# Performance work log

Hardware: AMD Instinct MI355X
Metric: run time of the kernel (lower is better)

The kernel has to match this reference:

```python
import jax, jax.numpy as jnp
import numpy as np

B, S, H, E, ID, ON, RF = 256, 512, 512, 128, 8192, 32, 32
RNN_IN = H + E + 1 + ON  # weighted + embedded + rate + online


def setup_inputs() -> dict:
    key = jax.random.key(0)
    ks = jax.random.split(key, 24)
    n = lambda k, sh, s=0.05: (jax.random.normal(k, sh, jnp.float32) * s)
    inp = {
        'input_id': jax.random.randint(ks[0], (B, 1), 0, ID),
        'input_rate': jax.random.uniform(ks[1], (B, 1), jnp.float32),
        'hidden': n(ks[2], (1, B, H), 1.0),
        'encoder_outputs': n(ks[3], (S, B, H), 1.0),
        'attn_mask': jax.random.randint(ks[4], (B, S), 0, 2).astype(jnp.float32),
        'pre_grid': jnp.zeros((B, 1), jnp.float32),
        'next_grid': jnp.zeros((B, 1), jnp.float32),
        'constraint_vec': jax.random.randint(ks[5], (B, ID), 0, 2).astype(jnp.float32),
        'pro_features': jnp.zeros((B, 8), jnp.float32),
        'online_features': n(ks[6], (B, ON), 1.0),
        'rid_features': n(ks[7], (B, RF), 1.0),
        # learned parameters
        'emb_id': n(ks[8], (ID, E)),
        'trans': n(ks[9], (ID, ID)),              # transition_matrix param
        'v_w': n(ks[10], (1, H)),                  # attention v (no bias)
        'attn_gate_w': n(ks[11], (H, 2 * H)),
        'attn_gate_b': jnp.zeros((H,), jnp.float32),
        'W_ih': n(ks[12], (3 * H, RNN_IN)),
        'W_hh': n(ks[13], (3 * H, H)),
        'b_ih': jnp.zeros((3 * H,), jnp.float32),
        'b_hh': jnp.zeros((3 * H,), jnp.float32),
        'gate_w': n(ks[14], (ID, ID)),             # Linear(id_size,id_size) of gate
        'gate_b': jnp.zeros((ID,), jnp.float32),
        'fc_id_w': n(ks[15], (ID, H)),
        'fc_id_b': jnp.zeros((ID,), jnp.float32),
        'tandem_w': n(ks[16], (H, E + H)),
        'tandem_b': jnp.zeros((H,), jnp.float32),
        'rate_w': n(ks[17], (1, H + RF)),
        'rate_b': jnp.zeros((1,), jnp.float32),
    }
    return inp


def reference(input_id, input_rate, hidden, encoder_outputs, attn_mask, pre_grid,
              next_grid, constraint_vec, pro_features, online_features, rid_features,
              emb_id, trans, v_w, attn_gate_w, attn_gate_b, W_ih, W_hh, b_ih, b_hh,
              gate_w, gate_b, fc_id_w, fc_id_b, tandem_w, tandem_b, rate_w, rate_b):
    h = hidden[0]                                  # [B,H]
    emb = emb_id[input_id[:, 0]]                   # [B,E] (dropout is eval no-op)

    # --- gated additive attention ---
    eo = jnp.transpose(encoder_outputs, (1, 0, 2))          # [B,S,H]
    hb = jnp.broadcast_to(h[:, None, :], eo.shape)          # [B,S,H]
    g = jax.nn.sigmoid(jnp.concatenate([hb, eo], -1) @ attn_gate_w.T + attn_gate_b)
    energy = jnp.tanh(g * hb + (1.0 - g) * eo)              # [B,S,H]
    att = jnp.squeeze(energy @ v_w.T, -1)                   # [B,S]
    att = jnp.where(attn_mask == 0, jnp.float32(-1e10), att)
    a = jax.nn.softmax(att, axis=1)
    weighted = jnp.einsum('bs,bsh->bh', a, eo)              # [B,H]

    # --- GRU cell (torch gate order r,z,n) ---
    rnn_in = jnp.concatenate([weighted, emb, input_rate, online_features], -1)
    gx = rnn_in @ W_ih.T + b_ih
    gh = h @ W_hh.T + b_hh
    r = jax.nn.sigmoid(gx[:, :H] + gh[:, :H])
    z = jax.nn.sigmoid(gx[:, H:2 * H] + gh[:, H:2 * H])
    nn_ = jnp.tanh(gx[:, 2 * H:] + r * gh[:, 2 * H:])
    h_new = (1.0 - z) * nn_ + z * h                          # [B,H]

    # --- gated transition matrix + masked log-softmax ---
    T = jax.nn.sigmoid(trans @ gate_w.T + gate_b)           # [ID,ID]
    logits = (h_new @ fc_id_w.T + fc_id_b) @ T              # [B,ID]
    maxes = jnp.max(logits, axis=1, keepdims=True) + 1e-5
    x_exp = jnp.exp(logits - maxes) * constraint_vec
    prediction_id = jnp.log(x_exp / jnp.sum(x_exp, axis=1, keepdims=True))

    # --- tandem rate head ---
    max_id = jnp.argmax(prediction_id, axis=1)
    id_emb = emb_id[max_id]
    rate_in = jax.nn.relu(jnp.concatenate([id_emb, h_new], -1) @ tandem_w.T + tandem_b)
    prediction_rate = jax.nn.sigmoid(
        jnp.concatenate([rate_in, rid_features], -1) @ rate_w.T + rate_b)
    return prediction_id, prediction_rate, h_new[None]
```

## Files before the change

### kernel.cpp

```cpp
#include <hip/hip_runtime.h>
#include <stdint.h>
#include <math.h>

#define B_    256
#define S_    512
#define H_    512
#define E_    128
#define ID_   8192
#define ON_   32
#define RF_   32
#define RIN_  673

typedef __attribute__((ext_vector_type(8))) short short8;
typedef __attribute__((ext_vector_type(4))) float f32x4;

__device__ __forceinline__ unsigned short f2bf(float x) {
    unsigned int u = __builtin_bit_cast(unsigned int, x);
    u += 0x7fffu + ((u >> 16) & 1u);
    return (unsigned short)(u >> 16);
}
__device__ __forceinline__ float bf2f(unsigned short v) {
    return __builtin_bit_cast(float, ((unsigned int)v) << 16);
}
__device__ __forceinline__ float sigf(float x) { return 1.0f / (1.0f + expf(-x)); }

__device__ __forceinline__ void async16(const void* g, void* l) {
    __builtin_amdgcn_global_load_lds((const __attribute__((address_space(1))) void*)g,
                                     (__attribute__((address_space(3))) void*)l, 16, 0, 0);
}

__global__ __launch_bounds__(256) void split_contig(const float* __restrict__ src,
        unsigned short* __restrict__ hi, unsigned short* __restrict__ lo, long long n4)
{
    long long i = (long long)blockIdx.x * 256 + threadIdx.x;
    if (i >= n4) return;
    float4 v = ((const float4*)src)[i];
    ushort4 h, l;
    h.x = f2bf(v.x); l.x = f2bf(v.x - bf2f(h.x));
    h.y = f2bf(v.y); l.y = f2bf(v.y - bf2f(h.y));
    h.z = f2bf(v.z); l.z = f2bf(v.z - bf2f(h.z));
    h.w = f2bf(v.w); l.w = f2bf(v.w - bf2f(h.w));
    ((ushort4*)hi)[i] = h;
    ((ushort4*)lo)[i] = l;
}

__global__ __launch_bounds__(256) void split_strided(const float* __restrict__ src,
        unsigned short* __restrict__ hi, unsigned short* __restrict__ lo,
        int rows, int cols, int stride, int coloff)
{
    int i = blockIdx.x * 256 + threadIdx.x;
    if (i >= rows * cols) return;
    int r = i / cols, c = i % cols;
    float v = src[(size_t)r * stride + coloff + c];
    unsigned short h = f2bf(v);
    hi[i] = h;
    lo[i] = f2bf(v - bf2f(h));
}

template<int BIAS , int ACT , int OSPLIT >
__global__ __launch_bounds__(256, 2) void gemm_split(
        const unsigned short* __restrict__ Ah, const unsigned short* __restrict__ Al,
        const unsigned short* __restrict__ Bh, const unsigned short* __restrict__ Bl,
        float* __restrict__ Cf, unsigned short* __restrict__ Ch, unsigned short* __restrict__ Cl,
        const float* __restrict__ bias, int M, int N, int K, int group_m)
{
    __shared__ short lds[2][16384];

    int num_m = M >> 7, num_n = N >> 7;
    int pid = blockIdx.x;
    int gsize = group_m * num_n;
    int gid = pid / gsize;
    int first_m = gid * group_m;
    int gsz = min(group_m, num_m - first_m);
    int bm = first_m + (pid % gsz);
    int bn = (pid % gsize) / gsz;
    int m0 = bm << 7, n0 = bn << 7;

    int tid = threadIdx.x;
    int w = tid >> 6, L = tid & 63;
    int wm = w & 1, wn = w >> 1;

    int ci0 = w * 128 + L;
    int ci1 = ci0 + 64;
    int row0 = ci0 >> 2, q0 = (ci0 & 3) ^ ((ci0 >> 3) & 3);
    int row1 = ci1 >> 2, q1 = (ci1 & 3) ^ ((ci1 >> 3) & 3);
    size_t aoff0 = (size_t)(m0 + row0) * K + q0 * 8;
    size_t aoff1 = (size_t)(m0 + row1) * K + q1 * 8;
    size_t boff0 = (size_t)(n0 + row0) * K + q0 * 8;
    size_t boff1 = (size_t)(n0 + row1) * K + q1 * 8;

    int r15 = L & 15;
    int qp = (L >> 4) ^ ((L >> 1) & 3);
    int fA = (wm * 64 + r15) * 32 + qp * 8;
    int fB = (wn * 64 + r15) * 32 + qp * 8;

    auto stage = [&](int buf) {
        short* l = &lds[buf][0];
        async16(Ah + aoff0, &l[ci0 * 8]);
        async16(Ah + aoff1, &l[ci1 * 8]);
        async16(Al + aoff0, &l[4096 + ci0 * 8]);
        async16(Al + aoff1, &l[4096 + ci1 * 8]);
        async16(Bh + boff0, &l[8192 + ci0 * 8]);
        async16(Bh + boff1, &l[8192 + ci1 * 8]);
        async16(Bl + boff0, &l[12288 + ci0 * 8]);
        async16(Bl + boff1, &l[12288 + ci1 * 8]);
        aoff0 += 32; aoff1 += 32; boff0 += 32; boff1 += 32;
    };

    f32x4 acc[4][4] = {};
    int nk = K >> 5;
    int cur = 0;

    stage(0);

    for (int t = 0; t < nk; ++t) {
        if (t + 1 < nk) {
            stage(cur ^ 1);
            asm volatile("s_waitcnt vmcnt(8)" ::: "memory");
        } else {
            asm volatile("s_waitcnt vmcnt(0)" ::: "memory");
        }
        __builtin_amdgcn_s_barrier();
        __builtin_amdgcn_sched_barrier(0);

        const short* l = &lds[cur][0];
        short8 fAh[4], fAl[4], fBh[4], fBl[4];
#pragma unroll
        for (int u = 0; u < 4; ++u) {
            fAh[u] = *(const short8*)&l[fA + u * 512];
            fAl[u] = *(const short8*)&l[4096 + fA + u * 512];
            fBh[u] = *(const short8*)&l[8192 + fB + u * 512];
            fBl[u] = *(const short8*)&l[12288 + fB + u * 512];
        }
#pragma unroll
        for (int mt = 0; mt < 4; ++mt)
#pragma unroll
            for (int nt = 0; nt < 4; ++nt) {
                acc[mt][nt] = __builtin_amdgcn_mfma_f32_16x16x32_bf16(fAh[mt], fBh[nt], acc[mt][nt], 0, 0, 0);
                acc[mt][nt] = __builtin_amdgcn_mfma_f32_16x16x32_bf16(fAh[mt], fBl[nt], acc[mt][nt], 0, 0, 0);
                acc[mt][nt] = __builtin_amdgcn_mfma_f32_16x16x32_bf16(fAl[mt], fBh[nt], acc[mt][nt], 0, 0, 0);
            }
        __builtin_amdgcn_sched_barrier(0);
        __builtin_amdgcn_s_barrier();
        __builtin_amdgcn_sched_barrier(0);
        cur ^= 1;
    }

    int rbase = (L >> 4) * 4;
    int cbase = L & 15;
#pragma unroll
    for (int mt = 0; mt < 4; ++mt) {
#pragma unroll
        for (int nt = 0; nt < 4; ++nt) {
#pragma unroll
            for (int r = 0; r < 4; ++r) {
                int row = m0 + wm * 64 + mt * 16 + rbase + r;
                int col = n0 + wn * 64 + nt * 16 + cbase;
                float v = acc[mt][nt][r];
                if (BIAS == 1) v += bias[row];
                if (BIAS == 2) v += bias[col];
                if (ACT == 1) v = sigf(v);
                size_t idx = (size_t)row * N + col;
                if (OSPLIT == 0) {
                    Cf[idx] = v;
                } else {
                    unsigned short h = f2bf(v);
                    Ch[idx] = h;
                    Cl[idx] = f2bf(v - bf2f(h));
                }
            }
        }
    }
}

template<int ACT >
__global__ __launch_bounds__(256) void small_gemm(const float* __restrict__ A, const float* __restrict__ B,
        const float* __restrict__ bias, float* __restrict__ C, int N, int K, int lda, int ldb)
{
    int m = blockIdx.y;
    int n = blockIdx.x * 256 + threadIdx.x;
    if (n >= N) return;
    const float* a = A + (size_t)m * lda;
    const float* b = B + (size_t)n * ldb;
    float s0 = 0.f, s1 = 0.f, s2 = 0.f, s3 = 0.f;
    int k = 0;
    for (; k + 4 <= K; k += 4) {
        s0 += a[k] * b[k];
        s1 += a[k + 1] * b[k + 1];
        s2 += a[k + 2] * b[k + 2];
        s3 += a[k + 3] * b[k + 3];
    }
    for (; k < K; ++k) s0 += a[k] * b[k];
    float v = (s0 + s1) + (s2 + s3);
    if (bias) v += bias[n];
    if (ACT == 2) v = fmaxf(v, 0.f);
    C[(size_t)m * N + n] = v;
}

__global__ __launch_bounds__(64) void attn_energy(const float* __restrict__ enc, const float* __restrict__ gpre,
        const float* __restrict__ hW1, const float* __restrict__ hid, const float* __restrict__ vw,
        float* __restrict__ att)
{
    int sb = blockIdx.x;
    int b = sb & (B_ - 1);
    int s = sb >> 8;
    int L = threadIdx.x;
    const float* e = enc + (size_t)sb * H_;
    const float* gp = gpre + (size_t)sb * H_;
    const float* hw = hW1 + (size_t)b * H_;
    const float* hb = hid + (size_t)b * H_;
    float sum = 0.f;
#pragma unroll
    for (int j = 0; j < 8; ++j) {
        int h = j * 64 + L;
        float eo = e[h];
        float g = sigf(gp[h] + hw[h]);
        float en = tanhf(g * hb[h] + (1.f - g) * eo);
        sum += en * vw[h];
    }
    for (int off = 32; off > 0; off >>= 1) sum += __shfl_down(sum, off);
    if (L == 0) att[(size_t)b * S_ + s] = sum;
}

__global__ __launch_bounds__(256) void softmax_weighted(const float* __restrict__ att, const float* __restrict__ mask,
        const float* __restrict__ enc, const float* __restrict__ emb_id, const int* __restrict__ input_id,
        const float* __restrict__ input_rate, const float* __restrict__ online, float* __restrict__ rnn_in)
{
    int b = blockIdx.x, t = threadIdx.x;
    __shared__ float a[S_];
    __shared__ float red[256];

    float v0 = att[(size_t)b * S_ + t];
    float v1 = att[(size_t)b * S_ + 256 + t];
    if (mask[(size_t)b * S_ + t] == 0.f) v0 = -1e10f;
    if (mask[(size_t)b * S_ + 256 + t] == 0.f) v1 = -1e10f;

    red[t] = fmaxf(v0, v1);
    __syncthreads();
    for (int s = 128; s > 0; s >>= 1) { if (t < s) red[t] = fmaxf(red[t], red[t + s]); __syncthreads(); }
    float mx = red[0];
    __syncthreads();

    float e0 = expf(v0 - mx), e1 = expf(v1 - mx);
    red[t] = e0 + e1;
    __syncthreads();
    for (int s = 128; s > 0; s >>= 1) { if (t < s) red[t] += red[t + s]; __syncthreads(); }
    float Z = red[0];
    a[t] = e0; a[t + 256] = e1;
    __syncthreads();

    float acc0 = 0.f, acc1 = 0.f;
    for (int s = 0; s < S_; ++s) {
        float as = a[s];
        const float* e = enc + ((size_t)s * B_ + b) * H_;
        acc0 += as * e[t];
        acc1 += as * e[t + 256];
    }
    float* rb = rnn_in + (size_t)b * RIN_;
    rb[t] = acc0 / Z;
    rb[256 + t] = acc1 / Z;
    if (t < E_) rb[H_ + t] = emb_id[(size_t)input_id[b] * E_ + t];
    else if (t == E_) rb[H_ + E_] = input_rate[b];
    else if (t < E_ + 1 + ON_) rb[H_ + E_ + 1 + (t - E_ - 1)] = online[(size_t)b * ON_ + (t - E_ - 1)];
}

__global__ __launch_bounds__(256) void gru_kernel(const float* __restrict__ gx, const float* __restrict__ gh,
        const float* __restrict__ hid, float* __restrict__ hnew)
{
    int i = blockIdx.x * 256 + threadIdx.x;
    int b = i >> 9, j = i & (H_ - 1);
    const float* gxb = gx + (size_t)b * 3 * H_;
    const float* ghb = gh + (size_t)b * 3 * H_;
    float r = sigf(gxb[j] + ghb[j]);
    float z = sigf(gxb[H_ + j] + ghb[H_ + j]);
    float nn = tanhf(gxb[2 * H_ + j] + r * ghb[2 * H_ + j]);
    hnew[i] = (1.f - z) * nn + z * hid[i];
}

__global__ __launch_bounds__(256) void pred_id_kernel(const float* __restrict__ logits, const float* __restrict__ cons,
        float* __restrict__ out, int* __restrict__ max_id)
{
    int b = blockIdx.x, t = threadIdx.x;
    const float* l = logits + (size_t)b * ID_;
    const float* c = cons + (size_t)b * ID_;
    __shared__ float red[256];
    __shared__ int redi[256];

    float mx = -INFINITY;
    for (int j = t; j < ID_; j += 256) mx = fmaxf(mx, l[j]);
    red[t] = mx;
    __syncthreads();
    for (int s = 128; s > 0; s >>= 1) { if (t < s) red[t] = fmaxf(red[t], red[t + s]); __syncthreads(); }
    float m = red[0] + 1e-5f;
    __syncthreads();

    float Z = 0.f;
    for (int j = t; j < ID_; j += 256) if (c[j] != 0.f) Z += expf(l[j] - m);
    red[t] = Z;
    __syncthreads();
    for (int s = 128; s > 0; s >>= 1) { if (t < s) red[t] += red[t + s]; __syncthreads(); }
    float lg = logf(red[0]);
    __syncthreads();

    float bv = -INFINITY; int bi = 0x7fffffff;
    for (int j = t; j < ID_; j += 256) {
        bool valid = (c[j] != 0.f);
        float p = valid ? (l[j] - m - lg) : -INFINITY;
        out[(size_t)b * ID_ + j] = valid ? p : -3.0e38f;
        if (p > bv) { bv = p; bi = j; }
    }
    red[t] = bv; redi[t] = bi;
    __syncthreads();
    for (int s = 128; s > 0; s >>= 1) {
        if (t < s) {
            float ov = red[t + s]; int oi = redi[t + s];
            if (ov > red[t] || (ov == red[t] && oi < redi[t])) { red[t] = ov; redi[t] = oi; }
        }
        __syncthreads();
    }
    if (t == 0) max_id[b] = (redi[0] == 0x7fffffff) ? 0 : redi[0];
}

__global__ __launch_bounds__(256) void tandem_in_kernel(const float* __restrict__ emb_id, const int* __restrict__ max_id,
        const float* __restrict__ hnew, float* __restrict__ tin)
{
    int i = blockIdx.x * 256 + threadIdx.x;
    int b = i / (E_ + H_), j = i - b * (E_ + H_);
    tin[i] = (j < E_) ? emb_id[(size_t)max_id[b] * E_ + j] : hnew[(size_t)b * H_ + (j - E_)];
}

__global__ __launch_bounds__(64) void rate_kernel(const float* __restrict__ rate_in, const float* __restrict__ rid,
        const float* __restrict__ rate_w, const float* __restrict__ rate_b, float* __restrict__ out)
{
    int b = blockIdx.x, L = threadIdx.x;
    float s = 0.f;
    for (int k = L; k < H_; k += 64) s += rate_in[(size_t)b * H_ + k] * rate_w[k];
    if (L < RF_) s += rid[(size_t)b * RF_ + L] * rate_w[H_ + L];
    for (int off = 32; off > 0; off >>= 1) s += __shfl_down(s, off);
    if (L == 0) out[b] = sigf(s + rate_b[0]);
}

extern "C" void kernel_launch(void* const* d_in, const int* in_sizes, int n_in,
                              void* d_out, int out_size, void* d_ws, size_t ws_size,
                              hipStream_t stream)
{
    (void)in_sizes; (void)n_in; (void)out_size; (void)ws_size;

    const int*   input_id   = (const int*)  d_in[0];
    const float* input_rate = (const float*)d_in[1];
    const float* hidden     = (const float*)d_in[2];
    const float* enc        = (const float*)d_in[3];
    const float* attn_mask  = (const float*)d_in[4];
    const float* constraint = (const float*)d_in[7];
    const float* online     = (const float*)d_in[9];
    const float* rid        = (const float*)d_in[10];
    const float* emb_id     = (const float*)d_in[11];
    const float* trans      = (const float*)d_in[12];
    const float* v_w        = (const float*)d_in[13];
    const float* agw        = (const float*)d_in[14];
    const float* agb        = (const float*)d_in[15];
    const float* W_ih       = (const float*)d_in[16];
    const float* W_hh       = (const float*)d_in[17];
    const float* b_ih       = (const float*)d_in[18];
    const float* b_hh       = (const float*)d_in[19];
    const float* gate_w     = (const float*)d_in[20];
    const float* gate_b     = (const float*)d_in[21];
    const float* fc_id_w    = (const float*)d_in[22];
    const float* fc_id_b    = (const float*)d_in[23];
    const float* tandem_w   = (const float*)d_in[24];
    const float* tandem_b   = (const float*)d_in[25];
    const float* rate_w     = (const float*)d_in[26];
    const float* rate_b     = (const float*)d_in[27];

    char* ws = (char*)d_ws;
    const size_t MB128 = 134217728ull;
    unsigned short* eoH  = (unsigned short*)(ws);
    unsigned short* eoL  = (unsigned short*)(ws + MB128);
    float*          gpre = (float*)        (ws + 2 * MB128);
    unsigned short* fwH = (unsigned short*)(ws);
    unsigned short* fwL = (unsigned short*)(ws + MB128);
    unsigned short* gwH = (unsigned short*)(ws);
    unsigned short* gwL = (unsigned short*)(ws + MB128);
    unsigned short* trH = (unsigned short*)(ws + 2 * MB128);
    unsigned short* trL = (unsigned short*)(ws + 3 * MB128);
    size_t o = 4 * MB128;
    auto alloc = [&](size_t bytes) { size_t cur = o; o += (bytes + 4095) & ~(size_t)4095; return cur; };
    unsigned short* TtH    = (unsigned short*)(ws + alloc(MB128));
    unsigned short* TtL    = (unsigned short*)(ws + alloc(MB128));
    unsigned short* W2H    = (unsigned short*)(ws + alloc((size_t)H_ * H_ * 2));
    unsigned short* W2L    = (unsigned short*)(ws + alloc((size_t)H_ * H_ * 2));
    float* hW1     = (float*)(ws + alloc((size_t)B_ * H_ * 4));
    float* att     = (float*)(ws + alloc((size_t)B_ * S_ * 4));
    float* rnn_in  = (float*)(ws + alloc((size_t)B_ * RIN_ * 4));
    float* gx      = (float*)(ws + alloc((size_t)B_ * 3 * H_ * 4));
    float* gh      = (float*)(ws + alloc((size_t)B_ * 3 * H_ * 4));
    float* logits1 = (float*)(ws + alloc((size_t)B_ * ID_ * 4));
    unsigned short* l1H = (unsigned short*)(ws + alloc((size_t)B_ * ID_ * 2));
    unsigned short* l1L = (unsigned short*)(ws + alloc((size_t)B_ * ID_ * 2));
    float* logits2 = (float*)(ws + alloc((size_t)B_ * ID_ * 4));
    float* tin     = (float*)(ws + alloc((size_t)B_ * (E_ + H_) * 4));
    float* rate_in = (float*)(ws + alloc((size_t)B_ * H_ * 4));
    int*   max_id  = (int*)  (ws + alloc((size_t)B_ * 4));

    unsigned short* hnH = (unsigned short*)logits1;
    unsigned short* hnL = (unsigned short*)logits1 + (size_t)B_ * H_;

    float* out  = (float*)d_out;
    float* rate_out = out + (size_t)B_ * ID_;
    float* hnew = out + (size_t)B_ * ID_ + B_;

    split_contig<<<(S_ * B_ * H_ / 4 + 255) / 256, 256, 0, stream>>>(enc, eoH, eoL, (long long)S_ * B_ * H_ / 4);
    split_strided<<<(H_ * H_ + 255) / 256, 256, 0, stream>>>(agw, W2H, W2L, H_, H_, 2 * H_, H_);
    gemm_split<0, 0, 0><<<(S_ * B_ / 128) * (H_ / 128), 256, 0, stream>>>(
        eoH, eoL, W2H, W2L, gpre, nullptr, nullptr, nullptr, S_ * B_, H_, H_, 8);
    small_gemm<0><<<dim3(2, B_), 256, 0, stream>>>(hidden, agw, agb, hW1, H_, H_, H_, 2 * H_);
    attn_energy<<<S_ * B_, 64, 0, stream>>>(enc, gpre, hW1, hidden, v_w, att);
    softmax_weighted<<<B_, 256, 0, stream>>>(att, attn_mask, enc, emb_id, input_id, input_rate, online, rnn_in);

    small_gemm<0><<<dim3(6, B_), 256, 0, stream>>>(rnn_in, W_ih, b_ih, gx, 3 * H_, RIN_, RIN_, RIN_);
    small_gemm<0><<<dim3(6, B_), 256, 0, stream>>>(hidden, W_hh, b_hh, gh, 3 * H_, H_, H_, H_);
    gru_kernel<<<B_ * H_ / 256, 256, 0, stream>>>(gx, gh, hidden, hnew);

    split_contig<<<(B_ * H_ / 4 + 255) / 256, 256, 0, stream>>>(hnew, hnH, hnL, (long long)B_ * H_ / 4);
    split_contig<<<((size_t)ID_ * H_ / 4 + 255) / 256, 256, 0, stream>>>(fc_id_w, fwH, fwL, (long long)ID_ * H_ / 4);
    gemm_split<2, 0, 1><<<(B_ / 128) * (ID_ / 128), 256, 0, stream>>>(
        hnH, hnL, fwH, fwL, nullptr, l1H, l1L, fc_id_b, B_, ID_, H_, 8);

    split_contig<<<((size_t)ID_ * ID_ / 4 + 255) / 256, 256, 0, stream>>>(gate_w, gwH, gwL, (long long)ID_ * ID_ / 4);
    split_contig<<<((size_t)ID_ * ID_ / 4 + 255) / 256, 256, 0, stream>>>(trans, trH, trL, (long long)ID_ * ID_ / 4);
    gemm_split<1, 1, 1><<<(ID_ / 128) * (ID_ / 128), 256, 0, stream>>>(
        gwH, gwL, trH, trL, nullptr, TtH, TtL, gate_b, ID_, ID_, ID_, 16);

    gemm_split<0, 0, 0><<<(B_ / 128) * (ID_ / 128), 256, 0, stream>>>(
        l1H, l1L, TtH, TtL, logits2, nullptr, nullptr, nullptr, B_, ID_, ID_, 8);

    pred_id_kernel<<<B_, 256, 0, stream>>>(logits2, constraint, out, max_id);

    tandem_in_kernel<<<B_ * (E_ + H_) / 256, 256, 0, stream>>>(emb_id, max_id, hnew, tin);
    small_gemm<2><<<dim3(2, B_), 256, 0, stream>>>(tin, tandem_w, tandem_b, rate_in, H_, E_ + H_, E_ + H_, E_ + H_);
    rate_kernel<<<B_, 64, 0, stream>>>(rate_in, rid, rate_w, rate_b, rate_out);
}
```

Measured before the change: 6.336 ms.

## Add 256x256-tile split-bf16 GEMM for the large ID×ID and encoder GEMMs

Adds a new 512-thread GEMM kernel with 256x256 output tiles (each wave computes 128x64) and double-buffered async LDS staging. It replaces the 128x128 kernel for the 8192x8192x8192 gate/transition GEMM and the encoder projection GEMM. Larger tiles raise arithmetic intensity per LDS byte and cut global traffic. The cost is 128 KB of LDS per block and many more accumulator registers, which can lower occupancy. The 8192 GEMM also has fewer blocks in flight than before.

```diff
diff --git a/kernel.cpp b/kernel.cpp
--- a/kernel.cpp
+++ b/kernel.cpp
@@ -155,6 +155,123 @@
 #pragma unroll
             for (int r = 0; r < 4; ++r) {
                 int row = m0 + wm * 64 + mt * 16 + rbase + r;
+                int col = n0 + wn * 64 + nt * 16 + cbase;
+                float v = acc[mt][nt][r];
+                if (BIAS == 1) v += bias[row];
+                if (BIAS == 2) v += bias[col];
+                if (ACT == 1) v = sigf(v);
+                size_t idx = (size_t)row * N + col;
+                if (OSPLIT == 0) {
+                    Cf[idx] = v;
+                } else {
+                    unsigned short h = f2bf(v);
+                    Ch[idx] = h;
+                    Cl[idx] = f2bf(v - bf2f(h));
+                }
+            }
+        }
+    }
+}
+
+template<int BIAS, int ACT, int OSPLIT>
+__global__ __launch_bounds__(512, 2) void gemm_split256(
+        const unsigned short* __restrict__ Ah, const unsigned short* __restrict__ Al,
+        const unsigned short* __restrict__ Bh, const unsigned short* __restrict__ Bl,
+        float* __restrict__ Cf, unsigned short* __restrict__ Ch, unsigned short* __restrict__ Cl,
+        const float* __restrict__ bias, int M, int N, int K, int group_m)
+{
+    __shared__ short lds[2][32768];
+
+    int num_m = M >> 8, num_n = N >> 8;
+    int pid = blockIdx.x;
+    int gsize = group_m * num_n;
+    int gid = pid / gsize;
+    int first_m = gid * group_m;
+    int gsz = min(group_m, num_m - first_m);
+    int bm = first_m + (pid % gsz);
+    int bn = (pid % gsize) / gsz;
+    int m0 = bm << 8, n0 = bn << 8;
+
+    int tid = threadIdx.x;
+    int w = tid >> 6, L = tid & 63;
+    int wm = w & 1, wn = w >> 1;
+
+    int ci0 = tid;
+    int ci1 = tid + 512;
+    int row0 = ci0 >> 2, q0 = (ci0 & 3) ^ ((ci0 >> 3) & 3);
+    int row1 = ci1 >> 2, q1 = (ci1 & 3) ^ ((ci1 >> 3) & 3);
+    size_t aoff0 = (size_t)(m0 + row0) * K + q0 * 8;
+    size_t aoff1 = (size_t)(m0 + row1) * K + q1 * 8;
+    size_t boff0 = (size_t)(n0 + row0) * K + q0 * 8;
+    size_t boff1 = (size_t)(n0 + row1) * K + q1 * 8;
+
+    int r15 = L & 15;
+    int qp = (L >> 4) ^ ((L >> 1) & 3);
+    int fA = (wm * 128 + r15) * 32 + qp * 8;
+    int fB = (wn * 64 + r15) * 32 + qp * 8;
+
+    auto stage = [&](int buf) {
+        short* l = &lds[buf][0];
+        async16(Ah + aoff0, &l[ci0 * 8]);
+        async16(Ah + aoff1, &l[ci1 * 8]);
+        async16(Al + aoff0, &l[8192 + ci0 * 8]);
+        async16(Al + aoff1, &l[8192 + ci1 * 8]);
+        async16(Bh + boff0, &l[16384 + ci0 * 8]);
+        async16(Bh + boff1, &l[16384 + ci1 * 8]);
+        async16(Bl + boff0, &l[24576 + ci0 * 8]);
+        async16(Bl + boff1, &l[24576 + ci1 * 8]);
+        aoff0 += 32; aoff1 += 32; boff0 += 32; boff1 += 32;
+    };
+
+    f32x4 acc[8][4] = {};
+    int nk = K >> 5;
+    int cur = 0;
+
+    stage(0);
+
+    for (int t = 0; t < nk; ++t) {
+        if (t + 1 < nk) {
+            stage(cur ^ 1);
+            asm volatile("s_waitcnt vmcnt(8)" ::: "memory");
+        } else {
+            asm volatile("s_waitcnt vmcnt(0)" ::: "memory");
+        }
+        __builtin_amdgcn_s_barrier();
+        __builtin_amdgcn_sched_barrier(0);
+
+        const short* l = &lds[cur][0];
+        short8 fBh[4], fBl[4];
+#pragma unroll
+        for (int u = 0; u < 4; ++u) {
+            fBh[u] = *(const short8*)&l[16384 + fB + u * 512];
+            fBl[u] = *(const short8*)&l[24576 + fB + u * 512];
+        }
+#pragma unroll
+        for (int mt = 0; mt < 8; ++mt) {
+            short8 a_h = *(const short8*)&l[fA + mt * 512];
+            short8 a_l = *(const short8*)&l[8192 + fA + mt * 512];
+#pragma unroll
+            for (int nt = 0; nt < 4; ++nt) {
+                acc[mt][nt] = __builtin_amdgcn_mfma_f32_16x16x32_bf16(a_h, fBh[nt], acc[mt][nt], 0, 0, 0);
+                acc[mt][nt] = __builtin_amdgcn_mfma_f32_16x16x32_bf16(a_h, fBl[nt], acc[mt][nt], 0, 0, 0);
+                acc[mt][nt] = __builtin_amdgcn_mfma_f32_16x16x32_bf16(a_l, fBh[nt], acc[mt][nt], 0, 0, 0);
+            }
+        }
+        __builtin_amdgcn_sched_barrier(0);
+        __builtin_amdgcn_s_barrier();
+        __builtin_amdgcn_sched_barrier(0);
+        cur ^= 1;
+    }
+
+    int rbase = (L >> 4) * 4;
+    int cbase = L & 15;
+#pragma unroll
+    for (int mt = 0; mt < 8; ++mt) {
+#pragma unroll
+        for (int nt = 0; nt < 4; ++nt) {
+#pragma unroll
+            for (int r = 0; r < 4; ++r) {
+                int row = m0 + wm * 128 + mt * 16 + rbase + r;
                 int col = n0 + wn * 64 + nt * 16 + cbase;
                 float v = acc[mt][nt][r];
                 if (BIAS == 1) v += bias[row];
@@ -411,7 +528,7 @@
 
     split_contig<<<(S_ * B_ * H_ / 4 + 255) / 256, 256, 0, stream>>>(enc, eoH, eoL, (long long)S_ * B_ * H_ / 4);
     split_strided<<<(H_ * H_ + 255) / 256, 256, 0, stream>>>(agw, W2H, W2L, H_, H_, 2 * H_, H_);
-    gemm_split<0, 0, 0><<<(S_ * B_ / 128) * (H_ / 128), 256, 0, stream>>>(
+    gemm_split256<0, 0, 0><<<(S_ * B_ / 256) * (H_ / 256), 512, 0, stream>>>(
         eoH, eoL, W2H, W2L, gpre, nullptr, nullptr, nullptr, S_ * B_, H_, H_, 8);
     small_gemm<0><<<dim3(2, B_), 256, 0, stream>>>(hidden, agw, agb, hW1, H_, H_, H_, 2 * H_);
     attn_energy<<<S_ * B_, 64, 0, stream>>>(enc, gpre, hW1, hidden, v_w, att);
@@ -428,8 +545,8 @@
 
     split_contig<<<((size_t)ID_ * ID_ / 4 + 255) / 256, 256, 0, stream>>>(gate_w, gwH, gwL, (long long)ID_ * ID_ / 4);
     split_contig<<<((size_t)ID_ * ID_ / 4 + 255) / 256, 256, 0, stream>>>(trans, trH, trL, (long long)ID_ * ID_ / 4);
-    gemm_split<1, 1, 1><<<(ID_ / 128) * (ID_ / 128), 256, 0, stream>>>(
-        gwH, gwL, trH, trL, nullptr, TtH, TtL, gate_b, ID_, ID_, ID_, 16);
+    gemm_split256<1, 1, 1><<<(ID_ / 256) * (ID_ / 256), 512, 0, stream>>>(
+        gwH, gwL, trH, trL, nullptr, TtH, TtL, gate_b, ID_, ID_, ID_, 8);
 
     gemm_split<0, 0, 0><<<(B_ / 128) * (ID_ / 128), 256, 0, stream>>>(
         l1H, l1L, TtH, TtL, logits2, nullptr, nullptr, nullptr, B_, ID_, ID_, 8);
```

Result: faster. 5.168 ms (-18.4%).
